# Kernel optimization log

Measured on AMD Instinct MI355X. Metric: run time of the kernel, lower is better.

The kernel has to match this reference:

```python
import jax, jax.numpy as jnp
import numpy as np

NUM_ROUTES = 2048
IN_CH = 32
NUM_CAPS = 32
OUT_CH = 32
NUM_ITER = 3
BATCH = 64


def setup_inputs() -> dict:
    key = jax.random.key(0)
    kx, kw = jax.random.split(key)
    x = jax.random.normal(kx, (BATCH, NUM_ROUTES, IN_CH), dtype=jnp.float32)
    # W matches nn.Parameter torch.randn(1, routes, caps, out, in); drop leading 1
    W = jax.random.normal(kw, (NUM_ROUTES, NUM_CAPS, OUT_CH, IN_CH), dtype=jnp.float32)
    return {"x": x, "W": W}


def _squash(s):
    # Faithful to original: norm taken over the trailing singleton dim,
    # i.e. elementwise: sq = s^2, out = sq*s / ((1+sq)*sqrt(sq))
    sq = s * s
    return sq * s / ((1.0 + sq) * jnp.sqrt(sq))


def reference(x, W):
    # u_hat[b,r,c,o] = W[r,c,o,:] @ x[b,r,:]
    u_hat = jnp.einsum('rcoi,bri->brco', W, x)  # [B,R,C,O]
    R, C = W.shape[0], W.shape[1]
    b_ij = jnp.zeros((R, C), dtype=x.dtype)
    v = None
    for it in range(NUM_ITER):
        c_ij = jax.nn.softmax(b_ij, axis=0)              # softmax over routes (dim=1 in torch)
        s = jnp.einsum('rc,brco->bco', c_ij, u_hat)      # [B,C,O]
        v = _squash(s)
        if it < NUM_ITER - 1:
            # agreement: <u_hat, v> over O, then batch-mean update of logits
            a = jnp.einsum('brco,bco->brc', u_hat, v)    # [B,R,C]
            b_ij = b_ij + a.mean(axis=0)
    return v[..., None]  # [B, num_capsules, out_channels, 1], matches v_j.squeeze(1)
```

## Files before the change

### kernel.cpp

```cpp
#include <hip/hip_runtime.h>
#include <hip/hip_bf16.h>


#define B_  64
#define R_  2048
#define CI  32
#define NC  32
#define OC  32
#define NCO 1024
#define RPB 8
#define GR  (R_ / RPB)
#define BN  65536

typedef __attribute__((ext_vector_type(8))) short bf16x8;
typedef __attribute__((ext_vector_type(4))) float f32x4;

static constexpr long WN = (long)R_ * NCO * CI;
static constexpr long XN = (long)B_ * R_ * CI;

__device__ __forceinline__ unsigned short rne_bf16(float f) {
  unsigned int u = __builtin_bit_cast(unsigned int, f);
  u += 0x7fffu + ((u >> 16) & 1u);
  return (unsigned short)(u >> 16);
}

__device__ __forceinline__ bf16x8 pack8(f32x4 a, f32x4 b) {
  bf16x8 r;
  r[0] = (short)rne_bf16(a[0]); r[1] = (short)rne_bf16(a[1]);
  r[2] = (short)rne_bf16(a[2]); r[3] = (short)rne_bf16(a[3]);
  r[4] = (short)rne_bf16(b[0]); r[5] = (short)rne_bf16(b[1]);
  r[6] = (short)rne_bf16(b[2]); r[7] = (short)rne_bf16(b[3]);
  return r;
}

__global__ __launch_bounds__(256) void cvt_kernel(const float* __restrict__ src,
                                                  unsigned short* __restrict__ dst,
                                                  int n4) {
  int i = blockIdx.x * blockDim.x + threadIdx.x;
  int stride = gridDim.x * blockDim.x;
  const f32x4* s4 = (const f32x4*)src;
  ushort4* d4 = (ushort4*)dst;
  for (; i < n4; i += stride) {
    f32x4 f = s4[i];
    ushort4 u;
    u.x = rne_bf16(f[0]); u.y = rne_bf16(f[1]);
    u.z = rne_bf16(f[2]); u.w = rne_bf16(f[3]);
    d4[i] = u;
  }
}

template<bool STORE_WB>
__global__ __launch_bounds__(256, 2) void s0_kernel(
    const float* __restrict__ x, const float* __restrict__ W,
    unsigned short* __restrict__ Wb,
    float* __restrict__ part) {
  const int tid  = threadIdx.x;
  const int lane = tid & 63;
  const int mw   = tid >> 6;
  const int g    = blockIdx.y;
  const int r0   = blockIdx.x * RPB;
  const int l15  = lane & 15;
  const int q    = lane >> 4;
  const int k0   = q * 8;
  const int bA   = mw * 16 + l15;

  f32x4 acc[16];
#pragma unroll
  for (int t = 0; t < 16; ++t) acc[t] = (f32x4){0.f, 0.f, 0.f, 0.f};

  for (int j = 0; j < RPB; ++j) {
    const int r = r0 + j;
    const f32x4* xp = (const f32x4*)(x + ((bA * R_ + r) * CI + k0));
    bf16x8 af = pack8(xp[0], xp[1]);
#pragma unroll
    for (int half = 0; half < 2; ++half) {
      f32x4 w0[8], w1[8];
#pragma unroll
      for (int tt = 0; tt < 8; ++tt) {
        const int t = half * 8 + tt;
        const int nrow = (g * 16 + t) * 16 + l15;
        const f32x4* wp = (const f32x4*)(W + (r * NCO + nrow) * CI + k0);
        w0[tt] = __builtin_nontemporal_load(wp);
        w1[tt] = __builtin_nontemporal_load(wp + 1);
      }
#pragma unroll
      for (int tt = 0; tt < 8; ++tt) {
        const int t = half * 8 + tt;
        const int nrow = (g * 16 + t) * 16 + l15;
        bf16x8 bfr = pack8(w0[tt], w1[tt]);
        if (STORE_WB && mw == (j & 3))
          *(bf16x8*)(Wb + (r * NCO + nrow) * CI + k0) = bfr;
        acc[t] = __builtin_amdgcn_mfma_f32_16x16x32_bf16(af, bfr, acc[t], 0, 0, 0);
      }
    }
  }
  const int pbase = blockIdx.x * BN;
#pragma unroll
  for (int t = 0; t < 16; ++t) {
    const int n = (g * 16 + t) * 16 + l15;
#pragma unroll
    for (int rr = 0; rr < 4; ++rr) {
      const int b = mw * 16 + q * 4 + rr;
      part[pbase + b * NCO + n] = acc[t][rr] * (1.0f / 2048.0f);
    }
  }
}

template<bool FAST>
__global__ __launch_bounds__(256, 3) void s_kernel(
    const float* __restrict__ x, const float* __restrict__ W,
    const unsigned short* __restrict__ xb, const unsigned short* __restrict__ Wb,
    const float* __restrict__ cmat,
    float* __restrict__ part) {
  const int tid  = threadIdx.x;
  const int lane = tid & 63;
  const int mw   = tid >> 6;
  const int g    = blockIdx.y;
  const int r0   = blockIdx.x * RPB;
  const int l15  = lane & 15;
  const int q    = lane >> 4;
  const int k0   = q * 8;
  const int bA   = mw * 16 + l15;

  f32x4 acc[16];
#pragma unroll
  for (int t = 0; t < 16; ++t) acc[t] = (f32x4){0.f, 0.f, 0.f, 0.f};
  const f32x4 zero4 = (f32x4){0.f, 0.f, 0.f, 0.f};

  for (int j = 0; j < RPB; ++j) {
    const int r = r0 + j;
    bf16x8 af;
    if (FAST) {
      af = *(const bf16x8*)(xb + ((bA * R_ + r) * CI + k0));
    } else {
      const f32x4* xp = (const f32x4*)(x + ((bA * R_ + r) * CI + k0));
      af = pack8(xp[0], xp[1]);
    }
    float cv[8];
#pragma unroll
    for (int cc = 0; cc < 8; ++cc) cv[cc] = cmat[(g * 8 + cc) * R_ + r];
#pragma unroll
    for (int half = 0; half < 2; ++half) {
      bf16x8 wf[8];
#pragma unroll
      for (int tt = 0; tt < 8; ++tt) {
        const int t = half * 8 + tt;
        const int nrow = (g * 16 + t) * 16 + l15;
        if (FAST) wf[tt] = *(const bf16x8*)(Wb + (r * NCO + nrow) * CI + k0);
        else {
          const f32x4* wp = (const f32x4*)(W + (r * NCO + nrow) * CI + k0);
          wf[tt] = pack8(wp[0], wp[1]);
        }
      }
#pragma unroll
      for (int tt = 0; tt < 8; ++tt) {
        const int t = half * 8 + tt;
        f32x4 u = __builtin_amdgcn_mfma_f32_16x16x32_bf16(af, wf[tt], zero4, 0, 0, 0);
        acc[t] += cv[t >> 1] * u;
      }
    }
  }
  const int pbase = blockIdx.x * BN;
#pragma unroll
  for (int t = 0; t < 16; ++t) {
    const int n = (g * 16 + t) * 16 + l15;
#pragma unroll
    for (int rr = 0; rr < 4; ++rr) {
      const int b = mw * 16 + q * 4 + rr;
      part[pbase + b * NCO + n] = acc[t][rr];
    }
  }
}

__global__ __launch_bounds__(256) void rs_kernel(const float* __restrict__ part,
                                                 float* __restrict__ o) {
  const int i = blockIdx.x * 256 + threadIdx.x;
  float a0 = 0.f, a1 = 0.f, a2 = 0.f, a3 = 0.f;
  for (int p = 0; p < GR; p += 4) {
    a0 += part[p * BN + i];
    a1 += part[(p + 1) * BN + i];
    a2 += part[(p + 2) * BN + i];
    a3 += part[(p + 3) * BN + i];
  }
  const float sv = (a0 + a1) + (a2 + a3);
  const float sq = sv * sv;
  o[i] = sq * sv / ((1.0f + sq) * sqrtf(sq));
}

template<bool FAST, bool FIRST>
__global__ __launch_bounds__(256, 3) void a_kernel(
    const float* __restrict__ x, const float* __restrict__ W,
    const unsigned short* __restrict__ xb, const unsigned short* __restrict__ Wb,
    const float* __restrict__ v,
    float* __restrict__ bb) {
  const int tid  = threadIdx.x;
  const int lane = tid & 63;
  const int mw   = tid >> 6;
  const int g    = blockIdx.y;
  const int r0   = blockIdx.x * RPB;
  const int l15  = lane & 15;
  const int q    = lane >> 4;
  const int k0   = q * 8;
  const int bA   = mw * 16 + l15;

  __shared__ float slab[4][32][65];
  __shared__ float accw[2][4][64];

  float vreg[16][4];
#pragma unroll
  for (int t = 0; t < 16; ++t) {
    const int n = (g * 16 + t) * 16 + l15;
#pragma unroll
    for (int rr = 0; rr < 4; ++rr)
      vreg[t][rr] = v[(mw * 16 + q * 4 + rr) * NCO + n];
  }
  const f32x4 zero4 = (f32x4){0.f, 0.f, 0.f, 0.f};

  for (int kk = 0; kk < 2; ++kk) {
#pragma unroll
    for (int jj = 0; jj < 4; ++jj) {
      const int r = r0 + kk * 4 + jj;
      bf16x8 af;
      if (FAST) {
        af = *(const bf16x8*)(xb + ((bA * R_ + r) * CI + k0));
      } else {
        const f32x4* xp = (const f32x4*)(x + ((bA * R_ + r) * CI + k0));
        af = pack8(xp[0], xp[1]);
      }
      float dotc[8];
#pragma unroll
      for (int cc = 0; cc < 8; ++cc) dotc[cc] = 0.f;
#pragma unroll
      for (int half = 0; half < 2; ++half) {
        bf16x8 wf[8];
#pragma unroll
        for (int tt = 0; tt < 8; ++tt) {
          const int t = half * 8 + tt;
          const int nrow = (g * 16 + t) * 16 + l15;
          if (FAST) wf[tt] = *(const bf16x8*)(Wb + (r * NCO + nrow) * CI + k0);
          else {
            const f32x4* wp = (const f32x4*)(W + (r * NCO + nrow) * CI + k0);
            wf[tt] = pack8(wp[0], wp[1]);
          }
        }
#pragma unroll
        for (int tt = 0; tt < 8; ++tt) {
          const int t = half * 8 + tt;
          f32x4 u = __builtin_amdgcn_mfma_f32_16x16x32_bf16(af, wf[tt], zero4, 0, 0, 0);
          dotc[t >> 1] += u[0] * vreg[t][0] + u[1] * vreg[t][1] +
                          u[2] * vreg[t][2] + u[3] * vreg[t][3];
        }
      }
#pragma unroll
      for (int cc = 0; cc < 8; ++cc)
        slab[mw][cc * 4 + jj][lane] = dotc[cc];
    }
    {
      const int p = lane >> 1, h = lane & 1;
      float sm = 0.f;
#pragma unroll
      for (int i = 0; i < 32; ++i) sm += slab[mw][p][h * 32 + i];
      accw[kk][mw][lane] = sm;
    }
  }
  __syncthreads();
  if (tid < 64) {
    const int kk = tid >> 5;
    const int p  = tid & 31;
    float tot = 0.f;
#pragma unroll
    for (int w = 0; w < 4; ++w)
      tot += accw[kk][w][p * 2] + accw[kk][w][p * 2 + 1];
    const int cc = p >> 2, jj = p & 3;
    const int r  = r0 + kk * 4 + jj;
    const int o  = (g * 8 + cc) * R_ + r;
    const float val = tot * (1.0f / 64.0f);
    bb[o] = FIRST ? val : (bb[o] + val);
  }
}

__global__ __launch_bounds__(256) void softmax_kernel(const float* __restrict__ bb,
                                                      float* __restrict__ cmat) {
  const int c = blockIdx.x;
  const int tid = threadIdx.x;
  __shared__ float red[8];
  float m = -1e30f;
  for (int r = tid; r < R_; r += 256) m = fmaxf(m, bb[c * R_ + r]);
#pragma unroll
  for (int s = 1; s < 64; s <<= 1) m = fmaxf(m, __shfl_xor(m, s));
  if ((tid & 63) == 0) red[tid >> 6] = m;
  __syncthreads();
  m = fmaxf(fmaxf(red[0], red[1]), fmaxf(red[2], red[3]));
  float sum = 0.f;
  for (int r = tid; r < R_; r += 256) sum += __expf(bb[c * R_ + r] - m);
#pragma unroll
  for (int s = 1; s < 64; s <<= 1) sum += __shfl_xor(sum, s);
  if ((tid & 63) == 0) red[4 + (tid >> 6)] = sum;
  __syncthreads();
  sum = red[4] + red[5] + red[6] + red[7];
  const float inv = 1.0f / sum;
  for (int r = tid; r < R_; r += 256)
    cmat[c * R_ + r] = __expf(bb[c * R_ + r] - m) * inv;
}

extern "C" void kernel_launch(void* const* d_in, const int* in_sizes, int n_in,
                              void* d_out, int out_size, void* d_ws, size_t ws_size,
                              hipStream_t stream) {
  const float* x = (const float*)d_in[0];
  const float* W = (const float*)d_in[1];
  float* out = (float*)d_out;

  char* ws = (char*)d_ws;
  float* bb   = (float*)(ws);
  float* cmat = (float*)(ws + (1 << 18));
  float* vbuf = (float*)(ws + 2 * (size_t)(1 << 18));
  float* part = (float*)(ws + (1 << 20));
  unsigned short* Wb = (unsigned short*)(ws + 65 * (size_t)(1 << 20));
  unsigned short* xb = (unsigned short*)(ws + 65 * (size_t)(1 << 20) + WN * 2);
  const size_t need_fast = 65 * (size_t)(1 << 20) + (size_t)WN * 2 + (size_t)XN * 2;
  const bool fast = ws_size >= need_fast;

  const dim3 grid(GR, 4);

  if (fast) {
    cvt_kernel<<<1024, 256, 0, stream>>>(x, xb, (int)(XN / 4));
    s0_kernel<true><<<grid, 256, 0, stream>>>(x, W, Wb, part);
  } else {
    s0_kernel<false><<<grid, 256, 0, stream>>>(x, W, Wb, part);
  }
  rs_kernel<<<256, 256, 0, stream>>>(part, vbuf);
  if (fast) a_kernel<true, true><<<grid, 256, 0, stream>>>(x, W, xb, Wb, vbuf, bb);
  else      a_kernel<false, true><<<grid, 256, 0, stream>>>(x, W, xb, Wb, vbuf, bb);
  softmax_kernel<<<NC, 256, 0, stream>>>(bb, cmat);
  if (fast) s_kernel<true><<<grid, 256, 0, stream>>>(x, W, xb, Wb, cmat, part);
  else      s_kernel<false><<<grid, 256, 0, stream>>>(x, W, xb, Wb, cmat, part);
  rs_kernel<<<256, 256, 0, stream>>>(part, vbuf);
  if (fast) a_kernel<true, false><<<grid, 256, 0, stream>>>(x, W, xb, Wb, vbuf, bb);
  else      a_kernel<false, false><<<grid, 256, 0, stream>>>(x, W, xb, Wb, vbuf, bb);
  softmax_kernel<<<NC, 256, 0, stream>>>(bb, cmat);
  if (fast) s_kernel<true><<<grid, 256, 0, stream>>>(x, W, xb, Wb, cmat, part);
  else      s_kernel<false><<<grid, 256, 0, stream>>>(x, W, xb, Wb, cmat, part);
  rs_kernel<<<256, 256, 0, stream>>>(part, out);
}
```

Baseline: 712.6 us.

## Retile routing kernels to 16 routes x 8 groups and split reduction into two passes

Doubles routes per block and halves the capsule slice per block (8 column groups of 128), which cuts the partial-sum buffer from 256 slices to 128 and lowers register use so occupancy can rise to 4 blocks. The fused first-iteration kernel that converted W while computing is replaced by a standalone W-to-bf16 conversion pass followed by a uniform-weight variant of s_kernel. The single long reduction becomes a two-stage vectorized reduce (16 slices, then 8). The trade-offs are an extra full read of fp32 W in a separate pass, an extra kernel launch per reduction, and more W reuse pressure per block.

```diff
diff --git a/kernel.cpp b/kernel.cpp
--- a/kernel.cpp
+++ b/kernel.cpp
@@ -1,5 +1,4 @@
 #include <hip/hip_runtime.h>
-#include <hip/hip_bf16.h>
 
 
 #define B_  64
@@ -8,8 +7,10 @@
 #define NC  32
 #define OC  32
 #define NCO 1024
-#define RPB 8
+#define RPB 16
 #define GR  (R_ / RPB)
+#define NG  8
+#define NSL 128
 #define BN  65536
 
 typedef __attribute__((ext_vector_type(8))) short bf16x8;
@@ -49,65 +50,22 @@
   }
 }
 
-template<bool STORE_WB>
-__global__ __launch_bounds__(256, 2) void s0_kernel(
-    const float* __restrict__ x, const float* __restrict__ W,
-    unsigned short* __restrict__ Wb,
-    float* __restrict__ part) {
-  const int tid  = threadIdx.x;
-  const int lane = tid & 63;
-  const int mw   = tid >> 6;
-  const int g    = blockIdx.y;
-  const int r0   = blockIdx.x * RPB;
-  const int l15  = lane & 15;
-  const int q    = lane >> 4;
-  const int k0   = q * 8;
-  const int bA   = mw * 16 + l15;
-
-  f32x4 acc[16];
-#pragma unroll
-  for (int t = 0; t < 16; ++t) acc[t] = (f32x4){0.f, 0.f, 0.f, 0.f};
-
-  for (int j = 0; j < RPB; ++j) {
-    const int r = r0 + j;
-    const f32x4* xp = (const f32x4*)(x + ((bA * R_ + r) * CI + k0));
-    bf16x8 af = pack8(xp[0], xp[1]);
-#pragma unroll
-    for (int half = 0; half < 2; ++half) {
-      f32x4 w0[8], w1[8];
-#pragma unroll
-      for (int tt = 0; tt < 8; ++tt) {
-        const int t = half * 8 + tt;
-        const int nrow = (g * 16 + t) * 16 + l15;
-        const f32x4* wp = (const f32x4*)(W + (r * NCO + nrow) * CI + k0);
-        w0[tt] = __builtin_nontemporal_load(wp);
-        w1[tt] = __builtin_nontemporal_load(wp + 1);
-      }
-#pragma unroll
-      for (int tt = 0; tt < 8; ++tt) {
-        const int t = half * 8 + tt;
-        const int nrow = (g * 16 + t) * 16 + l15;
-        bf16x8 bfr = pack8(w0[tt], w1[tt]);
-        if (STORE_WB && mw == (j & 3))
-          *(bf16x8*)(Wb + (r * NCO + nrow) * CI + k0) = bfr;
-        acc[t] = __builtin_amdgcn_mfma_f32_16x16x32_bf16(af, bfr, acc[t], 0, 0, 0);
-      }
-    }
-  }
-  const int pbase = blockIdx.x * BN;
-#pragma unroll
-  for (int t = 0; t < 16; ++t) {
-    const int n = (g * 16 + t) * 16 + l15;
-#pragma unroll
-    for (int rr = 0; rr < 4; ++rr) {
-      const int b = mw * 16 + q * 4 + rr;
-      part[pbase + b * NCO + n] = acc[t][rr] * (1.0f / 2048.0f);
-    }
-  }
-}
-
-template<bool FAST>
-__global__ __launch_bounds__(256, 3) void s_kernel(
+__global__ __launch_bounds__(256) void cvtW_kernel(const float* __restrict__ src,
+                                                   unsigned short* __restrict__ dst) {
+  long i = (long)blockIdx.x * 256 + threadIdx.x;
+  const long stride = (long)gridDim.x * 256;
+  const long n8 = WN / 8;
+  const f32x4* s4 = (const f32x4*)src;
+  bf16x8* d8 = (bf16x8*)dst;
+  for (; i < n8; i += stride) {
+    f32x4 a = __builtin_nontemporal_load(s4 + 2 * i);
+    f32x4 b = __builtin_nontemporal_load(s4 + 2 * i + 1);
+    d8[i] = pack8(a, b);
+  }
+}
+
+template<bool FAST, bool UNIFORM>
+__global__ __launch_bounds__(256, 4) void s_kernel(
     const float* __restrict__ x, const float* __restrict__ W,
     const unsigned short* __restrict__ xb, const unsigned short* __restrict__ Wb,
     const float* __restrict__ cmat,
@@ -122,9 +80,9 @@
   const int k0   = q * 8;
   const int bA   = mw * 16 + l15;
 
-  f32x4 acc[16];
-#pragma unroll
-  for (int t = 0; t < 16; ++t) acc[t] = (f32x4){0.f, 0.f, 0.f, 0.f};
+  f32x4 acc[8];
+#pragma unroll
+  for (int t = 0; t < 8; ++t) acc[t] = (f32x4){0.f, 0.f, 0.f, 0.f};
   const f32x4 zero4 = (f32x4){0.f, 0.f, 0.f, 0.f};
 
   for (int j = 0; j < RPB; ++j) {
@@ -136,59 +94,75 @@
       const f32x4* xp = (const f32x4*)(x + ((bA * R_ + r) * CI + k0));
       af = pack8(xp[0], xp[1]);
     }
-    float cv[8];
-#pragma unroll
-    for (int cc = 0; cc < 8; ++cc) cv[cc] = cmat[(g * 8 + cc) * R_ + r];
-#pragma unroll
-    for (int half = 0; half < 2; ++half) {
-      bf16x8 wf[8];
-#pragma unroll
-      for (int tt = 0; tt < 8; ++tt) {
-        const int t = half * 8 + tt;
-        const int nrow = (g * 16 + t) * 16 + l15;
-        if (FAST) wf[tt] = *(const bf16x8*)(Wb + (r * NCO + nrow) * CI + k0);
-        else {
-          const f32x4* wp = (const f32x4*)(W + (r * NCO + nrow) * CI + k0);
-          wf[tt] = pack8(wp[0], wp[1]);
-        }
-      }
-#pragma unroll
-      for (int tt = 0; tt < 8; ++tt) {
-        const int t = half * 8 + tt;
-        f32x4 u = __builtin_amdgcn_mfma_f32_16x16x32_bf16(af, wf[tt], zero4, 0, 0, 0);
+    bf16x8 wf[8];
+#pragma unroll
+    for (int t = 0; t < 8; ++t) {
+      const int nrow = g * NSL + t * 16 + l15;
+      const int wof = (r * NCO + nrow) * CI + k0;
+      if (FAST) wf[t] = *(const bf16x8*)(Wb + wof);
+      else {
+        const f32x4* wp = (const f32x4*)(W + wof);
+        wf[t] = pack8(wp[0], wp[1]);
+      }
+    }
+    if (UNIFORM) {
+#pragma unroll
+      for (int t = 0; t < 8; ++t)
+        acc[t] = __builtin_amdgcn_mfma_f32_16x16x32_bf16(af, wf[t], acc[t], 0, 0, 0);
+    } else {
+      float cv[4];
+#pragma unroll
+      for (int cc = 0; cc < 4; ++cc) cv[cc] = cmat[(g * 4 + cc) * R_ + r];
+#pragma unroll
+      for (int t = 0; t < 8; ++t) {
+        f32x4 u = __builtin_amdgcn_mfma_f32_16x16x32_bf16(af, wf[t], zero4, 0, 0, 0);
         acc[t] += cv[t >> 1] * u;
       }
     }
   }
   const int pbase = blockIdx.x * BN;
 #pragma unroll
-  for (int t = 0; t < 16; ++t) {
-    const int n = (g * 16 + t) * 16 + l15;
+  for (int t = 0; t < 8; ++t) {
+    const int n = g * NSL + t * 16 + l15;
 #pragma unroll
     for (int rr = 0; rr < 4; ++rr) {
       const int b = mw * 16 + q * 4 + rr;
-      part[pbase + b * NCO + n] = acc[t][rr];
-    }
-  }
-}
-
-__global__ __launch_bounds__(256) void rs_kernel(const float* __restrict__ part,
-                                                 float* __restrict__ o) {
-  const int i = blockIdx.x * 256 + threadIdx.x;
-  float a0 = 0.f, a1 = 0.f, a2 = 0.f, a3 = 0.f;
-  for (int p = 0; p < GR; p += 4) {
-    a0 += part[p * BN + i];
-    a1 += part[(p + 1) * BN + i];
-    a2 += part[(p + 2) * BN + i];
-    a3 += part[(p + 3) * BN + i];
-  }
-  const float sv = (a0 + a1) + (a2 + a3);
-  const float sq = sv * sv;
-  o[i] = sq * sv / ((1.0f + sq) * sqrtf(sq));
+      part[pbase + b * NCO + n] = UNIFORM ? acc[t][rr] * (1.0f / 2048.0f)
+                                          : acc[t][rr];
+    }
+  }
+}
+
+__global__ __launch_bounds__(256) void rs1_kernel(const float* __restrict__ part,
+                                                  float* __restrict__ part2) {
+  const int i4 = blockIdx.x * 256 + threadIdx.x;
+  const int ip = blockIdx.y;
+  const f32x4* p4 = (const f32x4*)part;
+  f32x4 s = (f32x4){0.f, 0.f, 0.f, 0.f};
+#pragma unroll
+  for (int p = 0; p < 16; ++p) s += p4[(ip * 16 + p) * (BN / 4) + i4];
+  ((f32x4*)part2)[ip * (BN / 4) + i4] = s;
+}
+
+__global__ __launch_bounds__(256) void rs2_kernel(const float* __restrict__ part2,
+                                                  float* __restrict__ o) {
+  const int i4 = blockIdx.x * 256 + threadIdx.x;
+  const f32x4* p4 = (const f32x4*)part2;
+  f32x4 s = (f32x4){0.f, 0.f, 0.f, 0.f};
+#pragma unroll
+  for (int ip = 0; ip < 8; ++ip) s += p4[ip * (BN / 4) + i4];
+  f32x4 r;
+#pragma unroll
+  for (int c = 0; c < 4; ++c) {
+    const float sv = s[c];
+    const float sq = sv * sv;
+    r[c] = sq * sv / ((1.0f + sq) * sqrtf(sq));
+  }
+  ((f32x4*)o)[i4] = r;
 }
 
 template<bool FAST, bool FIRST>
-__global__ __launch_bounds__(256, 3) void a_kernel(
+__global__ __launch_bounds__(256, 4) void a_kernel(
     const float* __restrict__ x, const float* __restrict__ W,
     const unsigned short* __restrict__ xb, const unsigned short* __restrict__ Wb,
     const float* __restrict__ v,
@@ -206,10 +180,10 @@
   __shared__ float slab[4][32][65];
   __shared__ float accw[2][4][64];
 
-  float vreg[16][4];
-#pragma unroll
-  for (int t = 0; t < 16; ++t) {
-    const int n = (g * 16 + t) * 16 + l15;
+  float vreg[8][4];
+#pragma unroll
+  for (int t = 0; t < 8; ++t) {
+    const int n = g * NSL + t * 16 + l15;
 #pragma unroll
     for (int rr = 0; rr < 4; ++rr)
       vreg[t][rr] = v[(mw * 16 + q * 4 + rr) * NCO + n];
@@ -217,9 +191,8 @@
   const f32x4 zero4 = (f32x4){0.f, 0.f, 0.f, 0.f};
 
   for (int kk = 0; kk < 2; ++kk) {
-#pragma unroll
-    for (int jj = 0; jj < 4; ++jj) {
-      const int r = r0 + kk * 4 + jj;
+    for (int jj = 0; jj < 8; ++jj) {
+      const int r = r0 + kk * 8 + jj;
       bf16x8 af;
       if (FAST) {
         af = *(const bf16x8*)(xb + ((bA * R_ + r) * CI + k0));
@@ -227,33 +200,27 @@
         const f32x4* xp = (const f32x4*)(x + ((bA * R_ + r) * CI + k0));
         af = pack8(xp[0], xp[1]);
       }
-      float dotc[8];
-#pragma unroll
-      for (int cc = 0; cc < 8; ++cc) dotc[cc] = 0.f;
-#pragma unroll
-      for (int half = 0; half < 2; ++half) {
-        bf16x8 wf[8];
-#pragma unroll
-        for (int tt = 0; tt < 8; ++tt) {
-          const int t = half * 8 + tt;
-          const int nrow = (g * 16 + t) * 16 + l15;
-          if (FAST) wf[tt] = *(const bf16x8*)(Wb + (r * NCO + nrow) * CI + k0);
-          else {
-            const f32x4* wp = (const f32x4*)(W + (r * NCO + nrow) * CI + k0);
-            wf[tt] = pack8(wp[0], wp[1]);
-          }
+      bf16x8 wf[8];
+#pragma unroll
+      for (int t = 0; t < 8; ++t) {
+        const int nrow = g * NSL + t * 16 + l15;
+        const int wof = (r * NCO + nrow) * CI + k0;
+        if (FAST) wf[t] = *(const bf16x8*)(Wb + wof);
+        else {
+          const f32x4* wp = (const f32x4*)(W + wof);
+          wf[t] = pack8(wp[0], wp[1]);
         }
-#pragma unroll
-        for (int tt = 0; tt < 8; ++tt) {
-          const int t = half * 8 + tt;
-          f32x4 u = __builtin_amdgcn_mfma_f32_16x16x32_bf16(af, wf[tt], zero4, 0, 0, 0);
-          dotc[t >> 1] += u[0] * vreg[t][0] + u[1] * vreg[t][1] +
-                          u[2] * vreg[t][2] + u[3] * vreg[t][3];
-        }
-      }
-#pragma unroll
-      for (int cc = 0; cc < 8; ++cc)
-        slab[mw][cc * 4 + jj][lane] = dotc[cc];
+      }
+      float dotc[4] = {0.f, 0.f, 0.f, 0.f};
+#pragma unroll
+      for (int t = 0; t < 8; ++t) {
+        f32x4 u = __builtin_amdgcn_mfma_f32_16x16x32_bf16(af, wf[t], zero4, 0, 0, 0);
+        dotc[t >> 1] += u[0] * vreg[t][0] + u[1] * vreg[t][1] +
+                        u[2] * vreg[t][2] + u[3] * vreg[t][3];
+      }
+#pragma unroll
+      for (int cc = 0; cc < 4; ++cc)
+        slab[mw][cc * 8 + jj][lane] = dotc[cc];
     }
     {
       const int p = lane >> 1, h = lane & 1;
@@ -271,9 +238,9 @@
 #pragma unroll
     for (int w = 0; w < 4; ++w)
       tot += accw[kk][w][p * 2] + accw[kk][w][p * 2 + 1];
-    const int cc = p >> 2, jj = p & 3;
-    const int r  = r0 + kk * 4 + jj;
-    const int o  = (g * 8 + cc) * R_ + r;
+    const int cc = p >> 3, jj = p & 7;
+    const int r  = r0 + kk * 8 + jj;
+    const int o  = (g * 4 + cc) * R_ + r;
     const float val = tot * (1.0f / 64.0f);
     bb[o] = FIRST ? val : (bb[o] + val);
   }
@@ -311,34 +278,42 @@
   float* out = (float*)d_out;
 
   char* ws = (char*)d_ws;
-  float* bb   = (float*)(ws);
-  float* cmat = (float*)(ws + (1 << 18));
-  float* vbuf = (float*)(ws + 2 * (size_t)(1 << 18));
-  float* part = (float*)(ws + (1 << 20));
-  unsigned short* Wb = (unsigned short*)(ws + 65 * (size_t)(1 << 20));
-  unsigned short* xb = (unsigned short*)(ws + 65 * (size_t)(1 << 20) + WN * 2);
-  const size_t need_fast = 65 * (size_t)(1 << 20) + (size_t)WN * 2 + (size_t)XN * 2;
+  float* bb    = (float*)(ws);
+  float* cmat  = (float*)(ws + (1 << 18));
+  float* vbuf  = (float*)(ws + 2 * (size_t)(1 << 18));
+  float* part2 = (float*)(ws + (1 << 20));
+  float* part  = (float*)(ws + 4 * (size_t)(1 << 20));
+  unsigned short* Wb = (unsigned short*)(ws + 36 * (size_t)(1 << 20));
+  unsigned short* xb = (unsigned short*)(ws + 36 * (size_t)(1 << 20) + WN * 2);
+  const size_t need_fast = 36 * (size_t)(1 << 20) + (size_t)WN * 2 + (size_t)XN * 2;
   const bool fast = ws_size >= need_fast;
 
-  const dim3 grid(GR, 4);
+  const dim3 grid(GR, NG);
+  const dim3 rgrid(BN / 1024, 8);
 
   if (fast) {
     cvt_kernel<<<1024, 256, 0, stream>>>(x, xb, (int)(XN / 4));
-    s0_kernel<true><<<grid, 256, 0, stream>>>(x, W, Wb, part);
+    cvtW_kernel<<<2048, 256, 0, stream>>>(W, Wb);
+    s_kernel<true, true><<<grid, 256, 0, stream>>>(x, W, xb, Wb, nullptr, part);
   } else {
-    s0_kernel<false><<<grid, 256, 0, stream>>>(x, W, Wb, part);
-  }
-  rs_kernel<<<256, 256, 0, stream>>>(part, vbuf);
+    s_kernel<false, true><<<grid, 256, 0, stream>>>(x, W, xb, Wb, nullptr, part);
+  }
+  rs1_kernel<<<rgrid, 256, 0, stream>>>(part, part2);
+  rs2_kernel<<<BN / 1024, 256, 0, stream>>>(part2, vbuf);
+
   if (fast) a_kernel<true, true><<<grid, 256, 0, stream>>>(x, W, xb, Wb, vbuf, bb);
   else      a_kernel<false, true><<<grid, 256, 0, stream>>>(x, W, xb, Wb, vbuf, bb);
   softmax_kernel<<<NC, 256, 0, stream>>>(bb, cmat);
-  if (fast) s_kernel<true><<<grid, 256, 0, stream>>>(x, W, xb, Wb, cmat, part);
-  else      s_kernel<false><<<grid, 256, 0, stream>>>(x, W, xb, Wb, cmat, part);
-  rs_kernel<<<256, 256, 0, stream>>>(part, vbuf);
+  if (fast) s_kernel<true, false><<<grid, 256, 0, stream>>>(x, W, xb, Wb, cmat, part);
+  else      s_kernel<false, false><<<grid, 256, 0, stream>>>(x, W, xb, Wb, cmat, part);
+  rs1_kernel<<<rgrid, 256, 0, stream>>>(part, part2);
+  rs2_kernel<<<BN / 1024, 256, 0, stream>>>(part2, vbuf);
+
   if (fast) a_kernel<true, false><<<grid, 256, 0, stream>>>(x, W, xb, Wb, vbuf, bb);
   else      a_kernel<false, false><<<grid, 256, 0, stream>>>(x, W, xb, Wb, vbuf, bb);
   softmax_kernel<<<NC, 256, 0, stream>>>(bb, cmat);
-  if (fast) s_kernel<true><<<grid, 256, 0, stream>>>(x, W, xb, Wb, cmat, part);
-  else      s_kernel<false><<<grid, 256, 0, stream>>>(x, W, xb, Wb, cmat, part);
-  rs_kernel<<<256, 256, 0, stream>>>(part, out);
-}
+  if (fast) s_kernel<true, false><<<grid, 256, 0, stream>>>(x, W, xb, Wb, cmat, part);
+  else      s_kernel<false, false><<<grid, 256, 0, stream>>>(x, W, xb, Wb, cmat, part);
+  rs1_kernel<<<rgrid, 256, 0, stream>>>(part, part2);
+  rs2_kernel<<<BN / 1024, 256, 0, stream>>>(part2, out);
+}
```

Measured after the change: 612.7 us. 1.16x faster.
